# Performance work log

Measured on AMD Instinct MI355X. Metric: run time of the kernel, lower is better.

## Reference

```python
import jax, jax.numpy as jnp
import numpy as np

N_NODES = 50000
N_EDGES = 1_600_000
F_IN = 128
HID = 64
HEADS = 4
NCLS = 2
NEG_SLOPE = 0.2  # PyG GATConv default


def setup_inputs() -> dict:
    key = jax.random.key(0)
    ks = jax.random.split(key, 12)
    s = 0.1
    return {
        "x": jax.random.normal(ks[0], (N_NODES, F_IN), jnp.float32),
        "edge_index": jax.random.randint(ks[1], (2, N_EDGES), 0, N_NODES, jnp.int32),
        "W1": jax.random.normal(ks[2], (F_IN, HEADS * HID), jnp.float32) * s,
        "att_src1": jax.random.normal(ks[3], (HEADS, HID), jnp.float32) * s,
        "att_dst1": jax.random.normal(ks[4], (HEADS, HID), jnp.float32) * s,
        "b1": jnp.zeros((HEADS * HID,), jnp.float32),
        "W2": jax.random.normal(ks[5], (HEADS * HID, HID), jnp.float32) * s,
        "att_src2": jax.random.normal(ks[6], (1, HID), jnp.float32) * s,
        "att_dst2": jax.random.normal(ks[7], (1, HID), jnp.float32) * s,
        "b2": jnp.zeros((HID,), jnp.float32),
        "Wc": jax.random.normal(ks[8], (HID, NCLS), jnp.float32) * s,
        "bc": jnp.zeros((NCLS,), jnp.float32),
    }


def _gat_layer(x, src, dst, W, a_src, a_dst, bias, heads, out_ch, concat):
    """Faithful PyG GATConv (eval mode): gather, LeakyReLU score, segment softmax by dst, scatter-add."""
    n = x.shape[0]
    h = (x @ W).reshape(n, heads, out_ch)            # [N, H, C]
    alpha_s = (h * a_src).sum(-1)                    # [N, H]
    alpha_d = (h * a_dst).sum(-1)                    # [N, H]
    e = jax.nn.leaky_relu(alpha_s[src] + alpha_d[dst], NEG_SLOPE)  # [E, H]
    e_max = jax.ops.segment_max(e, dst, num_segments=n)
    ex = jnp.exp(e - e_max[dst])
    denom = jax.ops.segment_sum(ex, dst, num_segments=n)
    coef = ex / (denom[dst] + 1e-16)                 # [E, H]
    out = jax.ops.segment_sum(h[src] * coef[:, :, None], dst, num_segments=n)  # [N, H, C]
    out = out.reshape(n, heads * out_ch) if concat else out.mean(axis=1)
    return out + bias


def reference(x, edge_index, W1, att_src1, att_dst1, b1, W2, att_src2, att_dst2, b2, Wc, bc):
    n = x.shape[0]
    loop = jnp.arange(n, dtype=edge_index.dtype)     # GATConv add_self_loops=True
    src = jnp.concatenate([edge_index[0], loop])
    dst = jnp.concatenate([edge_index[1], loop])
    h1 = jax.nn.elu(_gat_layer(x, src, dst, W1, att_src1, att_dst1, b1, HEADS, HID, True))
    # dropout p=0.6 is identity in eval mode
    h2 = jax.nn.elu(_gat_layer(h1, src, dst, W2, att_src2, att_dst2, b2, 1, HID, False))
    pooled = h2.mean(axis=0, keepdims=True)          # batch=None path: [1, HID]
    return pooled @ Wc + bc                          # [1, NCLS]
```

## Files before the change

kernel.cpp:

```cpp
#include <hip/hip_runtime.h>
#include <cstdint>
#include <cstddef>

#define NEG_SLOPE 0.2f
#define F_IN 128
#define C1 256
#define HID 64
#define HEADS 4
#define LOG2E 1.4426950408889634f
#define NBUCK 196
#define BCAP 10240

typedef __attribute__((ext_vector_type(8))) short bf16x8;
typedef __attribute__((ext_vector_type(4))) float f32x4;
typedef __attribute__((ext_vector_type(2))) float f32x2;
typedef unsigned long long ull;

__device__ __forceinline__ float wave_reduce_sum(float v) {
#pragma unroll
  for (int off = 32; off > 0; off >>= 1) v += __shfl_down(v, off);
  return v;
}

__device__ __forceinline__ unsigned short f2bf(float f) {
  union { float f; unsigned int u; } v; v.f = f;
  unsigned int u = v.u;
  unsigned int r = (u + 0x7fffu + ((u >> 16) & 1u)) >> 16;
  return (unsigned short)r;
}

__device__ __forceinline__ unsigned char f2fp8(float f) {
  int p = __builtin_amdgcn_cvt_pk_fp8_f32(f, f, 0, false);
  return (unsigned char)(p & 0xff);
}

__global__ __launch_bounds__(256) void setup_kernel(const float* __restrict__ W1,
                                                    const float* __restrict__ W2,
                                                    unsigned short* __restrict__ W1b,
                                                    unsigned short* __restrict__ W2b,
                                                    int* __restrict__ gcursor,
                                                    float* __restrict__ poolrep) {
  const int TOT = 256 + 4096 + 32768 + 16384;
  for (int idx = threadIdx.x + blockIdx.x * 256; idx < TOT; idx += 256 * gridDim.x) {
    if (idx < 256) {
      gcursor[idx] = 0;
    } else if (idx < 256 + 4096) {
      poolrep[idx - 256] = 0.f;
    } else if (idx < 256 + 4096 + 32768) {
      int o = idx - (256 + 4096);
      int head = o >> 13, ks = (o >> 11) & 3, nt = (o >> 9) & 3;
      int lane = (o >> 3) & 63, j = o & 7;
      int k = ks * 32 + (lane >> 4) * 8 + j;
      int c = head * 64 + nt * 16 + (lane & 15);
      W1b[o] = f2bf(W1[k * 256 + c]);
    } else {
      int o = idx - (256 + 4096 + 32768);
      int ks = o >> 11, nt = (o >> 9) & 3, lane = (o >> 3) & 63, j = o & 7;
      int k = ks * 32 + (lane >> 4) * 8 + j;
      int c = nt * 16 + (lane & 15);
      W2b[o] = f2bf(W2[k * 64 + c]);
    }
  }
}

__global__ __launch_bounds__(256) void gemm1_mfma(const float* __restrict__ Af,
                                                  const unsigned short* __restrict__ Wb,
                                                  unsigned char* __restrict__ H8,
                                                  float* __restrict__ as_out,
                                                  float* __restrict__ ad_out,
                                                  const float* __restrict__ att_s,
                                                  const float* __restrict__ att_d,
                                                  int M) {
  constexpr int KSTEPS = 4, NH = HEADS, K = 128, N = 256;
  const int lane = threadIdx.x & 63, wid = threadIdx.x >> 6;
  const int rowbase = blockIdx.x * 64 + wid * 16;
  const int g = lane >> 4, li = lane & 15;
  int r_a = rowbase + li;
  if (r_a > M - 1) r_a = M - 1;

  f32x4 acc[NH][4];
#pragma unroll
  for (int h = 0; h < NH; h++)
#pragma unroll
    for (int nt = 0; nt < 4; nt++) {
      acc[h][nt][0] = 0.f; acc[h][nt][1] = 0.f; acc[h][nt][2] = 0.f; acc[h][nt][3] = 0.f;
    }

#pragma unroll
  for (int ks = 0; ks < KSTEPS; ks++) {
    bf16x8 a;
    const float* p = Af + (size_t)r_a * K + ks * 32 + g * 8;
    float4 v0 = *(const float4*)p, v1 = *(const float4*)(p + 4);
    a[0] = (short)f2bf(v0.x); a[1] = (short)f2bf(v0.y);
    a[2] = (short)f2bf(v0.z); a[3] = (short)f2bf(v0.w);
    a[4] = (short)f2bf(v1.x); a[5] = (short)f2bf(v1.y);
    a[6] = (short)f2bf(v1.z); a[7] = (short)f2bf(v1.w);
#pragma unroll
    for (int h = 0; h < NH; h++)
#pragma unroll
      for (int nt = 0; nt < 4; nt++) {
        bf16x8 b = *(const bf16x8*)(Wb + ((size_t)((h * KSTEPS + ks) * 4 + nt) * 64 + lane) * 8);
        acc[h][nt] = __builtin_amdgcn_mfma_f32_16x16x32_bf16(a, b, acc[h][nt], 0, 0, 0);
      }
  }

#pragma unroll
  for (int h = 0; h < NH; h++) {
    float asum[4] = {0.f, 0.f, 0.f, 0.f}, dsum[4] = {0.f, 0.f, 0.f, 0.f};
#pragma unroll
    for (int nt = 0; nt < 4; nt++) {
      float ws = att_s[h * 64 + nt * 16 + li];
      float wd = att_d[h * 64 + nt * 16 + li];
#pragma unroll
      for (int r = 0; r < 4; r++) { asum[r] += acc[h][nt][r] * ws; dsum[r] += acc[h][nt][r] * wd; }
    }
#pragma unroll
    for (int r = 0; r < 4; r++) {
#pragma unroll
      for (int m = 1; m < 16; m <<= 1) {
        asum[r] += __shfl_xor(asum[r], m);
        dsum[r] += __shfl_xor(dsum[r], m);
      }
    }
#pragma unroll
    for (int r = 0; r < 4; r++) {
      int gr = rowbase + g * 4 + r;
      if (gr < M) {
#pragma unroll
        for (int nt = 0; nt < 4; nt++)
          H8[(size_t)gr * N + h * 64 + nt * 16 + li] = f2fp8(acc[h][nt][r]);
        if (li == 0) {
          as_out[(size_t)gr * NH + h] = asum[r] * LOG2E;
          ad_out[(size_t)gr * NH + h] = dsum[r] * LOG2E;
        }
      }
    }
  }
}

__global__ __launch_bounds__(256) void partition_kernel(const int* __restrict__ esrc,
                                                        const int* __restrict__ edst,
                                                        int* __restrict__ gcursor,
                                                        unsigned* __restrict__ pairs,
                                                        int E, int Etot) {
  __shared__ int hist[256];
  __shared__ int base[256];
  const int tid = threadIdx.x;
  const int e0 = blockIdx.x * 2048;
  hist[tid] = 0;
  __syncthreads();
  int d8[8], rk8[8], bk8[8];
#pragma unroll
  for (int j = 0; j < 8; j++) {
    int e = e0 + tid * 8 + j;
    d8[j] = -1;
    if (e < Etot) {
      int d = (e < E) ? edst[e] : (e - E);
      d8[j] = d;
      bk8[j] = d >> 8;
      rk8[j] = atomicAdd(&hist[bk8[j]], 1);
    }
  }
  __syncthreads();
  if (hist[tid] > 0) base[tid] = atomicAdd(&gcursor[tid], hist[tid]);
  __syncthreads();
#pragma unroll
  for (int j = 0; j < 8; j++) {
    int e = e0 + tid * 8 + j;
    if (e < Etot) {
      int s = (e < E) ? esrc[e] : (e - E);
      pairs[(size_t)bk8[j] * BCAP + base[bk8[j]] + rk8[j]] =
          (unsigned)s | ((unsigned)(d8[j] & 255) << 16);
    }
  }
}

__global__ __launch_bounds__(512) void bucket_csr(const unsigned* __restrict__ pairs,
                                                  const int* __restrict__ gcursor,
                                                  const float4* __restrict__ as1,
                                                  const float4* __restrict__ ad1,
                                                  unsigned short* __restrict__ src16,
                                                  ull* __restrict__ w4,
                                                  int* __restrict__ row_ptr,
                                                  int N, int Etot) {
  __shared__ int hist[256], offs[256], cnt2[256], gpre[256];
  const int b = blockIdx.x;
  const int tid = threadIdx.x;
  if (tid < 256) {
    hist[tid] = 0; cnt2[tid] = 0;
    gpre[tid] = (tid < NBUCK) ? gcursor[tid] : 0;
  }
  __syncthreads();
  for (int off = 1; off < 256; off <<= 1) {
    int t = 0;
    if (tid < 256 && tid >= off) t = gpre[tid - off];
    __syncthreads();
    if (tid < 256) gpre[tid] += t;
    __syncthreads();
  }
  const int cnt = gcursor[b];
  const int gbase = (b == 0) ? 0 : gpre[b - 1];
  const unsigned* bp = pairs + (size_t)b * BCAP;
  if (b == 0 && tid == 0) row_ptr[N] = Etot;

  for (int i = tid; i < cnt; i += 512) {
    unsigned p = bp[i];
    atomicAdd(&hist[p >> 16], 1);
  }
  __syncthreads();
  if (tid < 256) offs[tid] = hist[tid];
  __syncthreads();
  for (int off = 1; off < 256; off <<= 1) {
    int t = 0;
    if (tid < 256 && tid >= off) t = offs[tid - off];
    __syncthreads();
    if (tid < 256) offs[tid] += t;
    __syncthreads();
  }
  if (tid < 256) {
    int node = b * 256 + tid;
    if (node < N) row_ptr[node] = gbase + offs[tid] - hist[tid];
  }
  __syncthreads();
  for (int i = tid; i < cnt; i += 512) {
    unsigned p = bp[i];
    int lo = (int)(p >> 16);
    int src = (int)(p & 0xffffu);
    int rank = atomicAdd(&cnt2[lo], 1);
    int pos = gbase + offs[lo] - hist[lo] + rank;
    float4 a = as1[src], dd = ad1[b * 256 + lo];
    float s0 = a.x + dd.x, s1 = a.y + dd.y, s2 = a.z + dd.z, s3 = a.w + dd.w;
    float w0 = exp2f(fmaxf(s0, NEG_SLOPE * s0));
    float w1 = exp2f(fmaxf(s1, NEG_SLOPE * s1));
    float w2 = exp2f(fmaxf(s2, NEG_SLOPE * s2));
    float w3 = exp2f(fmaxf(s3, NEG_SLOPE * s3));
    unsigned w01 = (unsigned)f2bf(w0) | ((unsigned)f2bf(w1) << 16);
    unsigned w23 = (unsigned)f2bf(w2) | ((unsigned)f2bf(w3) << 16);
    src16[pos] = (unsigned short)src;
    w4[pos] = (ull)w01 | ((ull)w23 << 32);
  }
}

__global__ __launch_bounds__(256) void agg1_gemm2(const unsigned char* __restrict__ H8,
                                                  const unsigned short* __restrict__ src16,
                                                  const ull* __restrict__ w4,
                                                  const int* __restrict__ row_ptr,
                                                  const float* __restrict__ b1,
                                                  const unsigned short* __restrict__ W2b,
                                                  const float* __restrict__ att_s2,
                                                  const float* __restrict__ att_d2,
                                                  unsigned char* __restrict__ H2,
                                                  float* __restrict__ as2,
                                                  float* __restrict__ ad2, int n) {
  __shared__ unsigned char lds_h[16 * 512];
  __shared__ float pA[4][16], pD[4][16];
  const int tid = threadIdx.x;
  const int l = tid & 63, w = tid >> 6;
  const int dbase = blockIdx.x * 16;
  const int hh = l >> 4;
  const int shamt = (hh & 1) ? 0 : 16;
  const bool lowpair = hh < 2;
  const float4 bb = *(const float4*)(b1 + l * 4);

#define WSEL(wv) __uint_as_float((((lowpair) ? (unsigned)(wv) : (unsigned)((wv) >> 32)) << shamt) & 0xffff0000u)
#define ACCUM(wgt, u8)                                                     \
  {                                                                        \
    f32x2 lo_ = __builtin_amdgcn_cvt_pk_f32_fp8((int)(u8), false);         \
    f32x2 hi_ = __builtin_amdgcn_cvt_pk_f32_fp8((int)(u8), true);          \
    accA += lo_ * (wgt); accB += hi_ * (wgt);                              \
    denom += (wgt);                                                        \
  }
  for (int i = 0; i < 4; i++) {
    int dloc = w * 4 + i;
    int d = dbase + dloc;
    bool active = d < n;
    f32x2 accA = {0.f, 0.f}, accB = {0.f, 0.f};
    float denom = 0.f;
    if (active) {
      int e0 = __builtin_amdgcn_readfirstlane(row_ptr[d]);
      int e1 = __builtin_amdgcn_readfirstlane(row_ptr[d + 1]);
      int e = e0;
      for (; e + 3 < e1; e += 4) {
        unsigned s0 = src16[e];
        unsigned s1 = src16[e + 1];
        unsigned s2 = src16[e + 2];
        unsigned s3 = src16[e + 3];
        ull wv0 = w4[e];
        ull wv1 = w4[e + 1];
        ull wv2 = w4[e + 2];
        ull wv3 = w4[e + 3];
        unsigned u0 = *(const unsigned*)(H8 + (size_t)s0 * C1 + l * 4);
        unsigned u1 = *(const unsigned*)(H8 + (size_t)s1 * C1 + l * 4);
        unsigned u2 = *(const unsigned*)(H8 + (size_t)s2 * C1 + l * 4);
        unsigned u3 = *(const unsigned*)(H8 + (size_t)s3 * C1 + l * 4);
        float w0 = WSEL(wv0), w1 = WSEL(wv1), w2 = WSEL(wv2), w3 = WSEL(wv3);
        ACCUM(w0, u0) ACCUM(w1, u1) ACCUM(w2, u2) ACCUM(w3, u3)
      }
      for (; e < e1; e++) {
        unsigned s0 = src16[e];
        ull wv = w4[e];
        unsigned u = *(const unsigned*)(H8 + (size_t)s0 * C1 + l * 4);
        float wq = WSEL(wv);
        ACCUM(wq, u)
      }
    }
    float inv = 1.f / (denom + 1e-16f);
    float4 o;
    o.x = accA[0] * inv + bb.x; o.y = accA[1] * inv + bb.y;
    o.z = accB[0] * inv + bb.z; o.w = accB[1] * inv + bb.w;
    o.x = o.x > 0.f ? o.x : (__expf(o.x) - 1.f);
    o.y = o.y > 0.f ? o.y : (__expf(o.y) - 1.f);
    o.z = o.z > 0.f ? o.z : (__expf(o.z) - 1.f);
    o.w = o.w > 0.f ? o.w : (__expf(o.w) - 1.f);
    if (!active) { o.x = 0.f; o.y = 0.f; o.z = 0.f; o.w = 0.f; }
    uint2 pk;
    pk.x = (unsigned int)f2bf(o.x) | ((unsigned int)f2bf(o.y) << 16);
    pk.y = (unsigned int)f2bf(o.z) | ((unsigned int)f2bf(o.w) << 16);
    unsigned byte = (unsigned)(l * 8) ^ ((unsigned)(dloc & 7) << 4);
    *(uint2*)(lds_h + dloc * 512 + byte) = pk;
  }
#undef ACCUM
#undef WSEL
  __syncthreads();

  const int li2 = l & 15, g2 = l >> 4;
  f32x4 acc2;
  acc2[0] = 0.f; acc2[1] = 0.f; acc2[2] = 0.f; acc2[3] = 0.f;
#pragma unroll
  for (int ks = 0; ks < 8; ks++) {
    unsigned byte = (unsigned)((ks * 32 + g2 * 8) * 2) ^ ((unsigned)(li2 & 7) << 4);
    bf16x8 a = *(const bf16x8*)(lds_h + li2 * 512 + byte);
    bf16x8 b = *(const bf16x8*)(W2b + ((size_t)(ks * 4 + w) * 64 + l) * 8);
    acc2 = __builtin_amdgcn_mfma_f32_16x16x32_bf16(a, b, acc2, 0, 0, 0);
  }

  float ws = att_s2[w * 16 + li2], wd = att_d2[w * 16 + li2];
  float asum[4], dsum[4];
#pragma unroll
  for (int r = 0; r < 4; r++) { asum[r] = acc2[r] * ws; dsum[r] = acc2[r] * wd; }
#pragma unroll
  for (int r = 0; r < 4; r++) {
#pragma unroll
    for (int m = 1; m < 16; m <<= 1) {
      asum[r] += __shfl_xor(asum[r], m);
      dsum[r] += __shfl_xor(dsum[r], m);
    }
  }
#pragma unroll
  for (int r = 0; r < 4; r++) {
    int row = g2 * 4 + r;
    int d2 = dbase + row;
    if (d2 < n) H2[(size_t)d2 * HID + w * 16 + li2] = f2fp8(acc2[r]);
    if (li2 == 0) { pA[w][row] = asum[r]; pD[w][row] = dsum[r]; }
  }
  __syncthreads();
  if (tid < 16) {
    int d2 = dbase + tid;
    if (d2 < n) as2[d2] = (pA[0][tid] + pA[1][tid] + pA[2][tid] + pA[3][tid]) * LOG2E;
  } else if (tid < 32) {
    int row = tid - 16;
    int d2 = dbase + row;
    if (d2 < n) ad2[d2] = (pD[0][row] + pD[1][row] + pD[2][row] + pD[3][row]) * LOG2E;
  }
}

__global__ __launch_bounds__(256) void agg2_pool(const unsigned char* __restrict__ H2,
                                                 const float* __restrict__ as_,
                                                 const float* __restrict__ ad_,
                                                 const int* __restrict__ row_ptr,
                                                 const unsigned short* __restrict__ src16,
                                                 const float* __restrict__ b2,
                                                 float* __restrict__ poolrep, int n) {
  __shared__ float lds[4][64];
  int wid = threadIdx.x >> 6;
  int d = blockIdx.x * 4 + wid;
  int l = threadIdx.x & 63, q = l >> 4, li = l & 15;
  float ad = ad_[d];
  int e0 = row_ptr[d], e1 = row_ptr[d + 1];
  f32x2 accA = {0.f, 0.f}, accB = {0.f, 0.f};
  float denom = 0.f;
  for (int e = e0 + q; e < e1; e += 4) {
    int s = (int)src16[e];
    float sc = as_[s] + ad;
    float w = exp2f(fmaxf(sc, NEG_SLOPE * sc));
    denom += w;
    unsigned u = *(const unsigned*)(H2 + (size_t)s * HID + li * 4);
    f32x2 lo_ = __builtin_amdgcn_cvt_pk_f32_fp8((int)u, false);
    f32x2 hi_ = __builtin_amdgcn_cvt_pk_f32_fp8((int)u, true);
    accA += lo_ * w; accB += hi_ * w;
  }
#pragma unroll
  for (int m = 16; m <= 32; m <<= 1) {
    accA[0] += __shfl_xor(accA[0], m); accA[1] += __shfl_xor(accA[1], m);
    accB[0] += __shfl_xor(accB[0], m); accB[1] += __shfl_xor(accB[1], m);
    denom += __shfl_xor(denom, m);
  }
  if (q == 0) {
    float inv = 1.f / (denom + 1e-16f);
    float o[4] = {accA[0] * inv + b2[li * 4], accA[1] * inv + b2[li * 4 + 1],
                  accB[0] * inv + b2[li * 4 + 2], accB[1] * inv + b2[li * 4 + 3]};
#pragma unroll
    for (int j = 0; j < 4; j++) {
      float v = o[j];
      lds[wid][li * 4 + j] = v > 0.f ? v : (__expf(v) - 1.f);
    }
  }
  __syncthreads();
  if (threadIdx.x < 64) {
    int c = threadIdx.x;
    float v = lds[0][c] + lds[1][c] + lds[2][c] + lds[3][c];
    atomicAdd(&poolrep[(blockIdx.x & 63) * 64 + c], v);
  }
}

__global__ __launch_bounds__(64) void head_kernel(const float* __restrict__ poolrep,
                                                  const float* __restrict__ Wc,
                                                  const float* __restrict__ bc,
                                                  float* __restrict__ out, float inv_n) {
  int l = threadIdx.x;
  float p = 0.f;
  for (int k = 0; k < 64; k++) p += poolrep[k * 64 + l];
  p *= inv_n;
  float o0 = wave_reduce_sum(p * Wc[l * 2 + 0]);
  float o1 = wave_reduce_sum(p * Wc[l * 2 + 1]);
  if (l == 0) { out[0] = o0 + bc[0]; out[1] = o1 + bc[1]; }
}

static inline size_t align256(size_t x) { return (x + 255) & ~(size_t)255; }

extern "C" void kernel_launch(void* const* d_in, const int* in_sizes, int n_in,
                              void* d_out, int out_size, void* d_ws, size_t ws_size,
                              hipStream_t stream) {
  const float* x        = (const float*)d_in[0];
  const int*   ei       = (const int*)d_in[1];
  const float* W1       = (const float*)d_in[2];
  const float* att_src1 = (const float*)d_in[3];
  const float* att_dst1 = (const float*)d_in[4];
  const float* b1       = (const float*)d_in[5];
  const float* W2       = (const float*)d_in[6];
  const float* att_src2 = (const float*)d_in[7];
  const float* att_dst2 = (const float*)d_in[8];
  const float* b2       = (const float*)d_in[9];
  const float* Wc       = (const float*)d_in[10];
  const float* bc       = (const float*)d_in[11];
  float* out = (float*)d_out;

  const int N = in_sizes[0] / F_IN;
  const int E = in_sizes[1] / 2;
  const int Etot = E + N;
  const int* ei_src = ei;
  const int* ei_dst = ei + E;

  char* w = (char*)d_ws;
  size_t off = 0;
  unsigned char* h1b8 = (unsigned char*)(w + off); off += align256((size_t)N * C1);
  unsigned char* h2b8 = (unsigned char*)(w + off); off += align256((size_t)N * HID);
  float* as1   = (float*)(w + off); off += align256((size_t)N * HEADS * 4);
  float* ad1   = (float*)(w + off); off += align256((size_t)N * HEADS * 4);
  float* as2   = (float*)(w + off); off += align256((size_t)N * 4);
  float* ad2   = (float*)(w + off); off += align256((size_t)N * 4);
  int* row_ptr = (int*)(w + off);   off += align256((size_t)(N + 1) * 4);
  int* gcursor = (int*)(w + off);   off += align256(256 * 4);
  float* poolrep = (float*)(w + off); off += align256(64 * 64 * 4);
  unsigned short* W1b = (unsigned short*)(w + off); off += align256(32768 * 2);
  unsigned short* W2b = (unsigned short*)(w + off); off += align256(16384 * 2);
  unsigned* pairs = (unsigned*)(w + off); off += align256((size_t)NBUCK * BCAP * 4);
  unsigned short* src16 = (unsigned short*)(w + off); off += align256((size_t)Etot * 2);
  ull* w4      = (ull*)(w + off);   off += align256((size_t)Etot * 8);

  int nb4 = (N + 3) / 4;
  int rowblocks = (N + 63) / 64;
  int pblocks = (Etot + 2047) / 2048;
  int fblocks = (N + 15) / 16;

  setup_kernel<<<104, 256, 0, stream>>>(W1, W2, W1b, W2b, gcursor, poolrep);
  partition_kernel<<<pblocks, 256, 0, stream>>>(ei_src, ei_dst, gcursor, pairs, E, Etot);
  gemm1_mfma<<<rowblocks, 256, 0, stream>>>(x, W1b, h1b8, as1, ad1,
                                            att_src1, att_dst1, N);
  bucket_csr<<<NBUCK, 512, 0, stream>>>(pairs, gcursor,
                                        (const float4*)as1, (const float4*)ad1,
                                        src16, w4, row_ptr, N, Etot);
  agg1_gemm2<<<fblocks, 256, 0, stream>>>(h1b8, src16, w4, row_ptr, b1, W2b,
                                          att_src2, att_dst2, h2b8, as2, ad2, N);
  agg2_pool<<<nb4, 256, 0, stream>>>(h2b8, as2, ad2, row_ptr, src16, b2, poolrep, N);
  head_kernel<<<1, 64, 0, stream>>>(poolrep, Wc, bc, out, 1.0f / (float)N);
}
```

Baseline: 213.1 us.

## Merge gemm1 and edge partition into one launch; unroll aggregation loops deeper

The GEMM1 kernel and the edge-partition kernel are independent, so they are combined into one launch that splits work by block index. This removes a launch and lets the two run concurrently on the GPU. The layer-1 aggregation loop is also unrolled from 4 to 8 edges, and the layer-2 pooling loop handles two edges per lane per iteration, so more gathers are in flight. In exchange, register pressure rises and the fused kernel's resource use is set by the heavier GEMM path.

Measured after the change: 185.1 us. 1.15x faster.

```diff
diff --git a/kernel.cpp b/kernel.cpp
--- a/kernel.cpp
+++ b/kernel.cpp
@@ -63,114 +63,115 @@
   }
 }
 
-__global__ __launch_bounds__(256) void gemm1_mfma(const float* __restrict__ Af,
-                                                  const unsigned short* __restrict__ Wb,
-                                                  unsigned char* __restrict__ H8,
-                                                  float* __restrict__ as_out,
-                                                  float* __restrict__ ad_out,
-                                                  const float* __restrict__ att_s,
-                                                  const float* __restrict__ att_d,
-                                                  int M) {
-  constexpr int KSTEPS = 4, NH = HEADS, K = 128, N = 256;
-  const int lane = threadIdx.x & 63, wid = threadIdx.x >> 6;
-  const int rowbase = blockIdx.x * 64 + wid * 16;
-  const int g = lane >> 4, li = lane & 15;
-  int r_a = rowbase + li;
-  if (r_a > M - 1) r_a = M - 1;
-
-  f32x4 acc[NH][4];
-#pragma unroll
-  for (int h = 0; h < NH; h++)
-#pragma unroll
-    for (int nt = 0; nt < 4; nt++) {
-      acc[h][nt][0] = 0.f; acc[h][nt][1] = 0.f; acc[h][nt][2] = 0.f; acc[h][nt][3] = 0.f;
-    }
-
-#pragma unroll
-  for (int ks = 0; ks < KSTEPS; ks++) {
-    bf16x8 a;
-    const float* p = Af + (size_t)r_a * K + ks * 32 + g * 8;
-    float4 v0 = *(const float4*)p, v1 = *(const float4*)(p + 4);
-    a[0] = (short)f2bf(v0.x); a[1] = (short)f2bf(v0.y);
-    a[2] = (short)f2bf(v0.z); a[3] = (short)f2bf(v0.w);
-    a[4] = (short)f2bf(v1.x); a[5] = (short)f2bf(v1.y);
-    a[6] = (short)f2bf(v1.z); a[7] = (short)f2bf(v1.w);
-#pragma unroll
-    for (int h = 0; h < NH; h++)
-#pragma unroll
-      for (int nt = 0; nt < 4; nt++) {
-        bf16x8 b = *(const bf16x8*)(Wb + ((size_t)((h * KSTEPS + ks) * 4 + nt) * 64 + lane) * 8);
-        acc[h][nt] = __builtin_amdgcn_mfma_f32_16x16x32_bf16(a, b, acc[h][nt], 0, 0, 0);
-      }
-  }
-
-#pragma unroll
-  for (int h = 0; h < NH; h++) {
-    float asum[4] = {0.f, 0.f, 0.f, 0.f}, dsum[4] = {0.f, 0.f, 0.f, 0.f};
-#pragma unroll
-    for (int nt = 0; nt < 4; nt++) {
-      float ws = att_s[h * 64 + nt * 16 + li];
-      float wd = att_d[h * 64 + nt * 16 + li];
-#pragma unroll
-      for (int r = 0; r < 4; r++) { asum[r] += acc[h][nt][r] * ws; dsum[r] += acc[h][nt][r] * wd; }
-    }
-#pragma unroll
-    for (int r = 0; r < 4; r++) {
-#pragma unroll
-      for (int m = 1; m < 16; m <<= 1) {
-        asum[r] += __shfl_xor(asum[r], m);
-        dsum[r] += __shfl_xor(dsum[r], m);
-      }
-    }
-#pragma unroll
-    for (int r = 0; r < 4; r++) {
-      int gr = rowbase + g * 4 + r;
-      if (gr < M) {
-#pragma unroll
-        for (int nt = 0; nt < 4; nt++)
-          H8[(size_t)gr * N + h * 64 + nt * 16 + li] = f2fp8(acc[h][nt][r]);
-        if (li == 0) {
-          as_out[(size_t)gr * NH + h] = asum[r] * LOG2E;
-          ad_out[(size_t)gr * NH + h] = dsum[r] * LOG2E;
-        }
-      }
-    }
-  }
-}
-
-__global__ __launch_bounds__(256) void partition_kernel(const int* __restrict__ esrc,
-                                                        const int* __restrict__ edst,
-                                                        int* __restrict__ gcursor,
-                                                        unsigned* __restrict__ pairs,
-                                                        int E, int Etot) {
+__global__ __launch_bounds__(256) void gemm1_partition(const float* __restrict__ Af,
+                                                       const unsigned short* __restrict__ Wb,
+                                                       unsigned char* __restrict__ H8,
+                                                       float* __restrict__ as_out,
+                                                       float* __restrict__ ad_out,
+                                                       const float* __restrict__ att_s,
+                                                       const float* __restrict__ att_d,
+                                                       int M, int rowblocks,
+                                                       const int* __restrict__ esrc,
+                                                       const int* __restrict__ edst,
+                                                       int* __restrict__ gcursor,
+                                                       unsigned* __restrict__ pairs,
+                                                       int E, int Etot) {
   __shared__ int hist[256];
   __shared__ int base[256];
-  const int tid = threadIdx.x;
-  const int e0 = blockIdx.x * 2048;
-  hist[tid] = 0;
-  __syncthreads();
-  int d8[8], rk8[8], bk8[8];
-#pragma unroll
-  for (int j = 0; j < 8; j++) {
-    int e = e0 + tid * 8 + j;
-    d8[j] = -1;
-    if (e < Etot) {
-      int d = (e < E) ? edst[e] : (e - E);
-      d8[j] = d;
-      bk8[j] = d >> 8;
-      rk8[j] = atomicAdd(&hist[bk8[j]], 1);
-    }
-  }
-  __syncthreads();
-  if (hist[tid] > 0) base[tid] = atomicAdd(&gcursor[tid], hist[tid]);
-  __syncthreads();
-#pragma unroll
-  for (int j = 0; j < 8; j++) {
-    int e = e0 + tid * 8 + j;
-    if (e < Etot) {
-      int s = (e < E) ? esrc[e] : (e - E);
-      pairs[(size_t)bk8[j] * BCAP + base[bk8[j]] + rk8[j]] =
-          (unsigned)s | ((unsigned)(d8[j] & 255) << 16);
+  if (blockIdx.x < rowblocks) {
+    constexpr int KSTEPS = 4, NH = HEADS, K = 128, N = 256;
+    const int lane = threadIdx.x & 63, wid = threadIdx.x >> 6;
+    const int rowbase = blockIdx.x * 64 + wid * 16;
+    const int g = lane >> 4, li = lane & 15;
+    int r_a = rowbase + li;
+    if (r_a > M - 1) r_a = M - 1;
+
+    f32x4 acc[NH][4];
+#pragma unroll
+    for (int h = 0; h < NH; h++)
+#pragma unroll
+      for (int nt = 0; nt < 4; nt++) {
+        acc[h][nt][0] = 0.f; acc[h][nt][1] = 0.f; acc[h][nt][2] = 0.f; acc[h][nt][3] = 0.f;
+      }
+
+#pragma unroll
+    for (int ks = 0; ks < KSTEPS; ks++) {
+      bf16x8 a;
+      const float* p = Af + (size_t)r_a * K + ks * 32 + g * 8;
+      float4 v0 = *(const float4*)p, v1 = *(const float4*)(p + 4);
+      a[0] = (short)f2bf(v0.x); a[1] = (short)f2bf(v0.y);
+      a[2] = (short)f2bf(v0.z); a[3] = (short)f2bf(v0.w);
+      a[4] = (short)f2bf(v1.x); a[5] = (short)f2bf(v1.y);
+      a[6] = (short)f2bf(v1.z); a[7] = (short)f2bf(v1.w);
+#pragma unroll
+      for (int h = 0; h < NH; h++)
+#pragma unroll
+        for (int nt = 0; nt < 4; nt++) {
+          bf16x8 b = *(const bf16x8*)(Wb + ((size_t)((h * KSTEPS + ks) * 4 + nt) * 64 + lane) * 8);
+          acc[h][nt] = __builtin_amdgcn_mfma_f32_16x16x32_bf16(a, b, acc[h][nt], 0, 0, 0);
+        }
+    }
+
+#pragma unroll
+    for (int h = 0; h < NH; h++) {
+      float asum[4] = {0.f, 0.f, 0.f, 0.f}, dsum[4] = {0.f, 0.f, 0.f, 0.f};
+#pragma unroll
+      for (int nt = 0; nt < 4; nt++) {
+        float ws = att_s[h * 64 + nt * 16 + li];
+        float wd = att_d[h * 64 + nt * 16 + li];
+#pragma unroll
+        for (int r = 0; r < 4; r++) { asum[r] += acc[h][nt][r] * ws; dsum[r] += acc[h][nt][r] * wd; }
+      }
+#pragma unroll
+      for (int r = 0; r < 4; r++) {
+#pragma unroll
+        for (int m = 1; m < 16; m <<= 1) {
+          asum[r] += __shfl_xor(asum[r], m);
+          dsum[r] += __shfl_xor(dsum[r], m);
+        }
+      }
+#pragma unroll
+      for (int r = 0; r < 4; r++) {
+        int gr = rowbase + g * 4 + r;
+        if (gr < M) {
+#pragma unroll
+          for (int nt = 0; nt < 4; nt++)
+            H8[(size_t)gr * N + h * 64 + nt * 16 + li] = f2fp8(acc[h][nt][r]);
+          if (li == 0) {
+            as_out[(size_t)gr * NH + h] = asum[r] * LOG2E;
+            ad_out[(size_t)gr * NH + h] = dsum[r] * LOG2E;
+          }
+        }
+      }
+    }
+  } else {
+    const int tid = threadIdx.x;
+    const int e0 = (blockIdx.x - rowblocks) * 2048;
+    hist[tid] = 0;
+    __syncthreads();
+    int d8[8], rk8[8], bk8[8];
+#pragma unroll
+    for (int j = 0; j < 8; j++) {
+      int e = e0 + tid * 8 + j;
+      d8[j] = -1;
+      if (e < Etot) {
+        int d = (e < E) ? edst[e] : (e - E);
+        d8[j] = d;
+        bk8[j] = d >> 8;
+        rk8[j] = atomicAdd(&hist[bk8[j]], 1);
+      }
+    }
+    __syncthreads();
+    if (hist[tid] > 0) base[tid] = atomicAdd(&gcursor[tid], hist[tid]);
+    __syncthreads();
+#pragma unroll
+    for (int j = 0; j < 8; j++) {
+      int e = e0 + tid * 8 + j;
+      if (e < Etot) {
+        int s = (e < E) ? esrc[e] : (e - E);
+        pairs[(size_t)bk8[j] * BCAP + base[bk8[j]] + rk8[j]] =
+            (unsigned)s | ((unsigned)(d8[j] & 255) << 16);
+      }
     }
   }
 }
@@ -280,21 +281,25 @@
       int e0 = __builtin_amdgcn_readfirstlane(row_ptr[d]);
       int e1 = __builtin_amdgcn_readfirstlane(row_ptr[d + 1]);
       int e = e0;
-      for (; e + 3 < e1; e += 4) {
-        unsigned s0 = src16[e];
-        unsigned s1 = src16[e + 1];
-        unsigned s2 = src16[e + 2];
-        unsigned s3 = src16[e + 3];
-        ull wv0 = w4[e];
-        ull wv1 = w4[e + 1];
-        ull wv2 = w4[e + 2];
-        ull wv3 = w4[e + 3];
+      for (; e + 7 < e1; e += 8) {
+        unsigned s0 = src16[e],     s1 = src16[e + 1];
+        unsigned s2 = src16[e + 2], s3 = src16[e + 3];
+        unsigned s4 = src16[e + 4], s5 = src16[e + 5];
+        unsigned s6 = src16[e + 6], s7 = src16[e + 7];
+        ull wv0 = w4[e],     wv1 = w4[e + 1], wv2 = w4[e + 2], wv3 = w4[e + 3];
+        ull wv4 = w4[e + 4], wv5 = w4[e + 5], wv6 = w4[e + 6], wv7 = w4[e + 7];
         unsigned u0 = *(const unsigned*)(H8 + (size_t)s0 * C1 + l * 4);
         unsigned u1 = *(const unsigned*)(H8 + (size_t)s1 * C1 + l * 4);
         unsigned u2 = *(const unsigned*)(H8 + (size_t)s2 * C1 + l * 4);
         unsigned u3 = *(const unsigned*)(H8 + (size_t)s3 * C1 + l * 4);
+        unsigned u4 = *(const unsigned*)(H8 + (size_t)s4 * C1 + l * 4);
+        unsigned u5 = *(const unsigned*)(H8 + (size_t)s5 * C1 + l * 4);
+        unsigned u6 = *(const unsigned*)(H8 + (size_t)s6 * C1 + l * 4);
+        unsigned u7 = *(const unsigned*)(H8 + (size_t)s7 * C1 + l * 4);
         float w0 = WSEL(wv0), w1 = WSEL(wv1), w2 = WSEL(wv2), w3 = WSEL(wv3);
+        float w4_ = WSEL(wv4), w5 = WSEL(wv5), w6 = WSEL(wv6), w7 = WSEL(wv7);
         ACCUM(w0, u0) ACCUM(w1, u1) ACCUM(w2, u2) ACCUM(w3, u3)
+        ACCUM(w4_, u4) ACCUM(w5, u5) ACCUM(w6, u6) ACCUM(w7, u7)
       }
       for (; e < e1; e++) {
         unsigned s0 = src16[e];
@@ -379,7 +384,24 @@
   int e0 = row_ptr[d], e1 = row_ptr[d + 1];
   f32x2 accA = {0.f, 0.f}, accB = {0.f, 0.f};
   float denom = 0.f;
-  for (int e = e0 + q; e < e1; e += 4) {
+  int e = e0 + q;
+  for (; e + 4 < e1; e += 8) {
+    int sa = (int)src16[e];
+    int sb = (int)src16[e + 4];
+    float sca = as_[sa] + ad, scb = as_[sb] + ad;
+    float wa = exp2f(fmaxf(sca, NEG_SLOPE * sca));
+    float wb = exp2f(fmaxf(scb, NEG_SLOPE * scb));
+    unsigned ua = *(const unsigned*)(H2 + (size_t)sa * HID + li * 4);
+    unsigned ub = *(const unsigned*)(H2 + (size_t)sb * HID + li * 4);
+    f32x2 loa = __builtin_amdgcn_cvt_pk_f32_fp8((int)ua, false);
+    f32x2 hia = __builtin_amdgcn_cvt_pk_f32_fp8((int)ua, true);
+    f32x2 lob = __builtin_amdgcn_cvt_pk_f32_fp8((int)ub, false);
+    f32x2 hib = __builtin_amdgcn_cvt_pk_f32_fp8((int)ub, true);
+    accA += loa * wa; accB += hia * wa;
+    accA += lob * wb; accB += hib * wb;
+    denom += wa + wb;
+  }
+  for (; e < e1; e += 4) {
     int s = (int)src16[e];
     float sc = as_[s] + ad;
     float w = exp2f(fmaxf(sc, NEG_SLOPE * sc));
@@ -474,9 +496,9 @@
   int fblocks = (N + 15) / 16;
 
   setup_kernel<<<104, 256, 0, stream>>>(W1, W2, W1b, W2b, gcursor, poolrep);
-  partition_kernel<<<pblocks, 256, 0, stream>>>(ei_src, ei_dst, gcursor, pairs, E, Etot);
-  gemm1_mfma<<<rowblocks, 256, 0, stream>>>(x, W1b, h1b8, as1, ad1,
-                                            att_src1, att_dst1, N);
+  gemm1_partition<<<rowblocks + pblocks, 256, 0, stream>>>(
+      x, W1b, h1b8, as1, ad1, att_src1, att_dst1, N, rowblocks,
+      ei_src, ei_dst, gcursor, pairs, E, Etot);
   bucket_csr<<<NBUCK, 512, 0, stream>>>(pairs, gcursor,
                                         (const float4*)as1, (const float4*)ad1,
                                         src16, w4, row_ptr, N, Etot);
```
